# Kernel optimization log

Hardware: AMD Instinct MI355X
Metric: run time of the kernel (lower is better)

Reference implementation:

```python
import jax, jax.numpy as jnp
import numpy as np

N_TOK, BATCH, D, MEM, H, W = 196, 64, 256, 2048, 16, 16


def setup_inputs() -> dict:
    key = jax.random.key(0)
    ks = jax.random.split(key, 9)
    w_scale = 1.0 / np.sqrt(D)  # ~ Linear default init scale
    return {
        "input_tokens": jax.random.normal(ks[0], (N_TOK, BATCH, D), jnp.float32),
        "ch_memory": jax.random.normal(ks[1], (MEM, D), jnp.float32) * 0.1,
        "ch_wq": jax.random.normal(ks[2], (D, D), jnp.float32) * w_scale,
        "ch_wk": jax.random.normal(ks[3], (D, D), jnp.float32) * w_scale,
        "ch_wv": jax.random.normal(ks[4], (D, D), jnp.float32) * w_scale,
        "sp_memory": jax.random.normal(ks[5], (MEM, H, W), jnp.float32) * 0.1,
        "sp_wq": jax.random.normal(ks[6], (D, D), jnp.float32) * w_scale,
        "sp_wk": jax.random.normal(ks[7], (D, D), jnp.float32) * w_scale,
        "sp_wv": jax.random.normal(ks[8], (D, D), jnp.float32) * w_scale,
    }


def reference(input_tokens, ch_memory, ch_wq, ch_wk, ch_wv,
              sp_memory, sp_wq, sp_wk, sp_wv):
    n_tok, batch, d = input_tokens.shape
    hw = d  # spatial branch requires feature_dim == H*W
    x = input_tokens.reshape(n_tok * batch, d)  # [NB, D]

    # ---- Channel memory branch: dot-product softmax read ----
    q = x @ ch_wq.T                       # [NB, D]
    k = ch_memory @ ch_wk.T               # [M, D]
    v = ch_memory @ ch_wv.T               # [M, D]
    scores = (q @ k.T) * (1.0 / jnp.sqrt(jnp.float32(d)))  # [NB, M]
    att_c = jax.nn.softmax(scores, axis=-1)
    out_c = att_c @ v                     # [NB, D]

    # ---- Spatial memory branch: SSIM-score softmax read ----
    mem_flat = sp_memory.reshape(sp_memory.shape[0], hw)  # [M, HW]
    qf = x @ sp_wq.T                      # [NB, HW]
    kf = mem_flat @ sp_wk.T               # [M, HW]
    vf = mem_flat @ sp_wv.T               # [M, HW]

    q_mean = jnp.mean(qf, axis=1, keepdims=True)          # [NB, 1]
    k_mean = jnp.mean(kf, axis=1, keepdims=True)          # [M, 1]
    q_var = jnp.var(qf, axis=1, ddof=1, keepdims=True)    # unbiased, like torch.var
    k_var = jnp.var(kf, axis=1, ddof=1, keepdims=True)
    cov = ((qf - q_mean) @ (kf - k_mean).T) / jnp.float32(hw - 1)  # [NB, M]

    c1, c2 = 0.01, 0.03
    mean_prod = q_mean @ k_mean.T                          # [NB, M]
    numerator = (2.0 * mean_prod + c1) * (2.0 * cov + c2)
    denominator = (q_mean ** 2 + (k_mean.T) ** 2 + c1) * (q_var + k_var.T + c2)
    ssim = numerator / (denominator + 1e-8)                # [NB, M]

    att_s = jax.nn.softmax(ssim, axis=-1)
    out_s = att_s @ vf                     # [NB, HW] == [NB, D]

    return (out_c + out_s).reshape(n_tok, batch, d)
```

## Files before the change

### kernel.cpp

```cpp
#include <hip/hip_runtime.h>

#define NBQ 12544
#define DM  256
#define MM  2048

typedef __attribute__((ext_vector_type(8)))  __bf16 bf16x8;
typedef __attribute__((ext_vector_type(4)))  float  floatx4;

__device__ __forceinline__ ushort f2bf(float x) {
    unsigned u = __float_as_uint(x);
    u += 0x7fffu + ((u >> 16) & 1u);
    return (ushort)(u >> 16);
}
__device__ __forceinline__ float bf2f(ushort h) {
    return __uint_as_float(((unsigned)h) << 16);
}

__global__ __launch_bounds__(256) void gemm_proj_all(
    const float* __restrict__ x,      const float* __restrict__ ch_mem,
    const float* __restrict__ ch_wq,  const float* __restrict__ ch_wk,
    const float* __restrict__ ch_wv,  const float* __restrict__ sp_mem,
    const float* __restrict__ sp_wq,  const float* __restrict__ sp_wk,
    const float* __restrict__ sp_wv,
    ushort* __restrict__ Qb,  ushort* __restrict__ QFb,
    ushort* __restrict__ Kb,  ushort* __restrict__ KFb,
    ushort* __restrict__ Vtb, ushort* __restrict__ VFtb)
{
    __shared__ ushort As[64][72];
    __shared__ ushort W1s[64][72];
    __shared__ ushort W2s[64][72];

    int bid = blockIdx.x;
    const float* A; const float* W1; const float* W2;
    ushort* C1; ushort* C2; int nrows, trans2;
    if (bid < 784) {
        A = x; W1 = ch_wq; W2 = sp_wq; C1 = Qb; C2 = QFb; nrows = NBQ; trans2 = 0;
    } else if (bid < 912) {
        A = ch_mem; W1 = ch_wk; W2 = ch_wv; C1 = Kb; C2 = Vtb;
        nrows = MM; trans2 = 1; bid -= 784;
    } else {
        A = sp_mem; W1 = sp_wk; W2 = sp_wv; C1 = KFb; C2 = VFtb;
        nrows = MM; trans2 = 1; bid -= 912;
    }
    const int r0 = (bid >> 2) * 64;
    const int c0 = (bid & 3) * 64;

    const int tid  = threadIdx.x;
    const int wv   = tid >> 6;
    const int lane = tid & 63;
    const int quad = lane >> 4;
    const int l16  = lane & 15;
    const int rw = (wv & 1) * 32;
    const int cw = (wv >> 1) * 32;

    floatx4 acc1[2][2], acc2[2][2];
    #pragma unroll
    for (int i = 0; i < 2; ++i)
        #pragma unroll
        for (int j = 0; j < 2; ++j) {
            acc1[i][j] = (floatx4){0.f, 0.f, 0.f, 0.f};
            acc2[i][j] = (floatx4){0.f, 0.f, 0.f, 0.f};
        }

    for (int d0 = 0; d0 < 256; d0 += 64) {
        __syncthreads();
        #pragma unroll
        for (int it = 0; it < 4; ++it) {
            int idx = tid + it * 256;
            int r = idx >> 4, c4 = (idx & 15) * 4;
            float4 a4 = *(const float4*)(A  + (size_t)(r0 + r) * 256 + d0 + c4);
            float4 w14 = *(const float4*)(W1 + (size_t)(c0 + r) * 256 + d0 + c4);
            float4 w24 = *(const float4*)(W2 + (size_t)(c0 + r) * 256 + d0 + c4);
            ushort4 ab, w1b, w2b;
            ab.x = f2bf(a4.x);  ab.y = f2bf(a4.y);  ab.z = f2bf(a4.z);  ab.w = f2bf(a4.w);
            w1b.x = f2bf(w14.x); w1b.y = f2bf(w14.y); w1b.z = f2bf(w14.z); w1b.w = f2bf(w14.w);
            w2b.x = f2bf(w24.x); w2b.y = f2bf(w24.y); w2b.z = f2bf(w24.z); w2b.w = f2bf(w24.w);
            *(ushort4*)&As[r][c4]  = ab;
            *(ushort4*)&W1s[r][c4] = w1b;
            *(ushort4*)&W2s[r][c4] = w2b;
        }
        __syncthreads();
        #pragma unroll
        for (int kk = 0; kk < 64; kk += 32) {
            bf16x8 aA0 = *(const bf16x8*)&As[rw + l16][kk + quad * 8];
            bf16x8 aA1 = *(const bf16x8*)&As[rw + 16 + l16][kk + quad * 8];
            bf16x8 b10 = *(const bf16x8*)&W1s[cw + l16][kk + quad * 8];
            bf16x8 b11 = *(const bf16x8*)&W1s[cw + 16 + l16][kk + quad * 8];
            bf16x8 b20 = *(const bf16x8*)&W2s[cw + l16][kk + quad * 8];
            bf16x8 b21 = *(const bf16x8*)&W2s[cw + 16 + l16][kk + quad * 8];
            acc1[0][0] = __builtin_amdgcn_mfma_f32_16x16x32_bf16(aA0, b10, acc1[0][0], 0, 0, 0);
            acc1[0][1] = __builtin_amdgcn_mfma_f32_16x16x32_bf16(aA0, b11, acc1[0][1], 0, 0, 0);
            acc1[1][0] = __builtin_amdgcn_mfma_f32_16x16x32_bf16(aA1, b10, acc1[1][0], 0, 0, 0);
            acc1[1][1] = __builtin_amdgcn_mfma_f32_16x16x32_bf16(aA1, b11, acc1[1][1], 0, 0, 0);
            acc2[0][0] = __builtin_amdgcn_mfma_f32_16x16x32_bf16(aA0, b20, acc2[0][0], 0, 0, 0);
            acc2[0][1] = __builtin_amdgcn_mfma_f32_16x16x32_bf16(aA0, b21, acc2[0][1], 0, 0, 0);
            acc2[1][0] = __builtin_amdgcn_mfma_f32_16x16x32_bf16(aA1, b20, acc2[1][0], 0, 0, 0);
            acc2[1][1] = __builtin_amdgcn_mfma_f32_16x16x32_bf16(aA1, b21, acc2[1][1], 0, 0, 0);
        }
    }

    #pragma unroll
    for (int ag = 0; ag < 2; ++ag)
        #pragma unroll
        for (int cg = 0; cg < 2; ++cg)
            #pragma unroll
            for (int i = 0; i < 4; ++i)
                C1[(size_t)(r0 + rw + ag * 16 + quad * 4 + i) * 256
                   + c0 + cw + cg * 16 + l16] = f2bf(acc1[ag][cg][i]);

    if (!trans2) {
        #pragma unroll
        for (int ag = 0; ag < 2; ++ag)
            #pragma unroll
            for (int cg = 0; cg < 2; ++cg)
                #pragma unroll
                for (int i = 0; i < 4; ++i)
                    C2[(size_t)(r0 + rw + ag * 16 + quad * 4 + i) * 256
                       + c0 + cw + cg * 16 + l16] = f2bf(acc2[ag][cg][i]);
    } else {
        __syncthreads();
        #pragma unroll
        for (int ag = 0; ag < 2; ++ag)
            #pragma unroll
            for (int cg = 0; cg < 2; ++cg)
                #pragma unroll
                for (int i = 0; i < 4; ++i)
                    W2s[cw + cg * 16 + l16][rw + ag * 16 + quad * 4 + i] = f2bf(acc2[ag][cg][i]);
        __syncthreads();
        const int col = tid >> 2;
        const int seg = (tid & 3) * 16;
        #pragma unroll
        for (int j = 0; j < 2; ++j)
            *(uint4*)(C2 + (size_t)(c0 + col) * nrows + r0 + seg + j * 8) =
                *(const uint4*)&W2s[col][seg + j * 8];
    }
}

__global__ __launch_bounds__(256) void row_stats_kf(
    const ushort* __restrict__ KFb, float* __restrict__ km, float* __restrict__ kv)
{
    const int row  = blockIdx.x * 4 + (threadIdx.x >> 6);
    const int lane = threadIdx.x & 63;
    ushort4 u = *(const ushort4*)(KFb + (size_t)row * 256 + lane * 4);
    float a = bf2f(u.x), b = bf2f(u.y), c = bf2f(u.z), d = bf2f(u.w);
    float s  = a + b + c + d;
    float ss = a * a + b * b + c * c + d * d;
    #pragma unroll
    for (int off = 32; off > 0; off >>= 1) {
        s  += __shfl_down(s, off);
        ss += __shfl_down(ss, off);
    }
    if (lane == 0) {
        float m = s * (1.f / 256.f);
        km[row] = m;
        kv[row] = (ss - 256.f * m * m) * (1.f / 255.f);
    }
}

__global__ __launch_bounds__(256, 2) void fused_attn_st(
    const ushort* __restrict__ Qb,  const ushort* __restrict__ QFb,
    const ushort* __restrict__ Kb,  const ushort* __restrict__ KFb,
    const ushort* __restrict__ Vtb, const ushort* __restrict__ VFtb,
    const float* __restrict__ km_, const float* __restrict__ kv_,
    float* __restrict__ out)
{
    __shared__ ushort SM[37376];
    ushort (*K_lds)[264]  = (ushort(*)[264])(SM);
    ushort (*KF_lds)[264] = (ushort(*)[264])(SM + 8448);
    ushort (*Vt_lds)[40]  = (ushort(*)[40])(SM + 16896);
    ushort (*VFt_lds)[40] = (ushort(*)[40])(SM + 27136);
    float* combuf = (float*)(SM + 16896);

    const int tid  = threadIdx.x;
    const int wv   = tid >> 6;
    const int lane = tid & 63;
    const int quad = lane >> 4;
    const int l16  = lane & 15;
    const int qsel = wv & 1;
    const int br   = wv >> 1;
    const int q0   = blockIdx.x * 32;

    const ushort* qsrc = br ? QFb : Qb;
    bf16x8 aQ[8];
    {
        const ushort* qp = qsrc + (size_t)(q0 + qsel * 16 + l16) * DM + quad * 8;
        #pragma unroll
        for (int s = 0; s < 8; ++s) aQ[s] = *(const bf16x8*)(qp + s * 32);
    }

    float qmv = 0.f, qvv = 0.f;
    if (br) {
        float sum = 0.f, ss = 0.f;
        #pragma unroll
        for (int s = 0; s < 8; ++s)
            #pragma unroll
            for (int j = 0; j < 8; ++j) {
                float v = (float)aQ[s][j];
                sum += v; ss += v * v;
            }
        sum += __shfl_xor(sum, 16, 64); sum += __shfl_xor(sum, 32, 64);
        ss  += __shfl_xor(ss, 16, 64);  ss  += __shfl_xor(ss, 32, 64);
        qmv = sum * (1.f / 256.f);
        qvv = (ss - 256.f * qmv * qmv) * (1.f / 255.f);
    }

    floatx4 acc[16];
    #pragma unroll
    for (int t = 0; t < 16; ++t) acc[t] = (floatx4){0.f, 0.f, 0.f, 0.f};
    float den = 0.f;

    for (int kt = 0; kt < MM; kt += 32) {
        __syncthreads();
        #pragma unroll
        for (int it = 0; it < 4; ++it) {
            int idx = tid + it * 256;
            int r = idx >> 5, c8 = (idx & 31) * 8;
            int pr = ((r & 4) << 2) | ((r >> 3) << 2) | (r & 3);
            *(uint4*)&K_lds[pr][c8]  = *(const uint4*)(Kb  + (size_t)(kt + r) * DM + c8);
            *(uint4*)&KF_lds[pr][c8] = *(const uint4*)(KFb + (size_t)(kt + r) * DM + c8);
        }
        #pragma unroll
        for (int it = 0; it < 4; ++it) {
            int idx = tid + it * 256;
            int d = idx >> 2, kc = (idx & 3) * 8;
            *(uint4*)&Vt_lds[d][kc]  = *(const uint4*)(Vtb  + (size_t)d * MM + kt + kc);
            *(uint4*)&VFt_lds[d][kc] = *(const uint4*)(VFtb + (size_t)d * MM + kt + kc);
        }
        __syncthreads();

        floatx4 S0 = (floatx4){0.f, 0.f, 0.f, 0.f};
        floatx4 S1 = (floatx4){0.f, 0.f, 0.f, 0.f};
        const ushort (*Ksrc)[264] = br ? KF_lds : K_lds;
        #pragma unroll
        for (int s = 0; s < 8; ++s) {
            bf16x8 aK0 = *(const bf16x8*)&Ksrc[l16][s * 32 + quad * 8];
            bf16x8 aK1 = *(const bf16x8*)&Ksrc[16 + l16][s * 32 + quad * 8];
            S0 = __builtin_amdgcn_mfma_f32_16x16x32_bf16(aK0, aQ[s], S0, 0, 0, 0);
            S1 = __builtin_amdgcn_mfma_f32_16x16x32_bf16(aK1, aQ[s], S1, 0, 0, 0);
        }

        float p[8];
        if (!br) {
            #pragma unroll
            for (int r = 0; r < 4; ++r) {
                p[r]     = __expf(S0[r] * 0.0625f);
                p[4 + r] = __expf(S1[r] * 0.0625f);
            }
        } else {
            floatx4 km0 = *(const floatx4*)(km_ + kt + 8 * quad);
            floatx4 km1 = *(const floatx4*)(km_ + kt + 8 * quad + 4);
            floatx4 kv0 = *(const floatx4*)(kv_ + kt + 8 * quad);
            floatx4 kv1 = *(const floatx4*)(kv_ + kt + 8 * quad + 4);
            #pragma unroll
            for (int r = 0; r < 4; ++r) {
                {
                    float mp  = qmv * km0[r];
                    float cov = (S0[r] - 256.f * mp) * (1.f / 255.f);
                    float num = (2.f * mp + 0.01f) * (2.f * cov + 0.03f);
                    float dn  = (qmv * qmv + km0[r] * km0[r] + 0.01f) * (qvv + kv0[r] + 0.03f);
                    p[r] = __expf(num / (dn + 1e-8f));
                }
                {
                    float mp  = qmv * km1[r];
                    float cov = (S1[r] - 256.f * mp) * (1.f / 255.f);
                    float num = (2.f * mp + 0.01f) * (2.f * cov + 0.03f);
                    float dn  = (qmv * qmv + km1[r] * km1[r] + 0.01f) * (qvv + kv1[r] + 0.03f);
                    p[4 + r] = __expf(num / (dn + 1e-8f));
                }
            }
        }
        union { ushort u[8]; bf16x8 v; } ap;
        #pragma unroll
        for (int j = 0; j < 8; ++j) {
            den += p[j];
            ap.u[j] = f2bf(p[j]);
        }

        const ushort (*Vsrc)[40] = br ? VFt_lds : Vt_lds;
        #pragma unroll
        for (int t = 0; t < 16; ++t) {
            bf16x8 bV = *(const bf16x8*)&Vsrc[t * 16 + l16][quad * 8];
            acc[t] = __builtin_amdgcn_mfma_f32_16x16x32_bf16(ap.v, bV, acc[t], 0, 0, 0);
        }
    }

    den += __shfl_xor(den, 16, 64);
    den += __shfl_xor(den, 32, 64);
    float rdn[4];
    #pragma unroll
    for (int r = 0; r < 4; ++r)
        rdn[r] = 1.f / __shfl(den, quad * 4 + r, 64);

    __syncthreads();
    if (br) {
        #pragma unroll
        for (int t = 0; t < 16; ++t)
            #pragma unroll
            for (int r = 0; r < 4; ++r)
                combuf[(qsel * 16 + quad * 4 + r) * 256 + t * 16 + l16] = acc[t][r] * rdn[r];
    }
    __syncthreads();
    if (!br) {
        #pragma unroll
        for (int t = 0; t < 16; ++t)
            #pragma unroll
            for (int r = 0; r < 4; ++r) {
                int ql = qsel * 16 + quad * 4 + r;
                out[(size_t)(q0 + ql) * DM + t * 16 + l16] =
                    acc[t][r] * rdn[r] + combuf[ql * 256 + t * 16 + l16];
            }
    }
}

extern "C" void kernel_launch(void* const* d_in, const int* in_sizes, int n_in,
                              void* d_out, int out_size, void* d_ws, size_t ws_size,
                              hipStream_t stream)
{
    const float* x      = (const float*)d_in[0];
    const float* ch_mem = (const float*)d_in[1];
    const float* ch_wq  = (const float*)d_in[2];
    const float* ch_wk  = (const float*)d_in[3];
    const float* ch_wv  = (const float*)d_in[4];
    const float* sp_mem = (const float*)d_in[5];
    const float* sp_wq  = (const float*)d_in[6];
    const float* sp_wk  = (const float*)d_in[7];
    const float* sp_wv  = (const float*)d_in[8];
    float* out = (float*)d_out;

    ushort* Qb   = (ushort*)d_ws;
    ushort* QFb  = Qb   + (size_t)NBQ * DM;
    ushort* Kb   = QFb  + (size_t)NBQ * DM;
    ushort* KFb  = Kb   + (size_t)MM * DM;
    ushort* Vtb  = KFb  + (size_t)MM * DM;
    ushort* VFtb = Vtb  + (size_t)MM * DM;
    float*  km   = (float*)(VFtb + (size_t)MM * DM);
    float*  kv   = km + MM;

    dim3 blk(256);
    gemm_proj_all<<<dim3(1040), blk, 0, stream>>>(
        x, ch_mem, ch_wq, ch_wk, ch_wv, sp_mem, sp_wq, sp_wk, sp_wv,
        Qb, QFb, Kb, KFb, Vtb, VFtb);
    row_stats_kf<<<dim3(MM / 4), blk, 0, stream>>>(KFb, km, kv);
    fused_attn_st<<<dim3(NBQ / 32), blk, 0, stream>>>(
        Qb, QFb, Kb, KFb, Vtb, VFtb, km, kv, out);
}
```

Baseline: 267.0 us.

## Fuse key row statistics into projection kernel with full-width row blocks

The projection kernel now gives each block 64 rows across all 256 output columns. The bf16 A tile is staged once in LDS and reused across the four column chunks, where before it was reloaded per column tile. For the spatial-memory keys, per-row sum and sum of squares are reduced from the accumulators inside the kernel, so the separate row_stats kernel and its launch go away. The grid shrinks from 1040 to 260 larger blocks, which lowers parallelism on the GPU. The stats now come from fp32 accumulators instead of the bf16-rounded stored values.

Measured after the change: 269.9 us. No clear change (+1.1%).

```diff
diff --git a/kernel.cpp b/kernel.cpp
--- a/kernel.cpp
+++ b/kernel.cpp
@@ -16,34 +16,37 @@
     return __uint_as_float(((unsigned)h) << 16);
 }
 
-__global__ __launch_bounds__(256) void gemm_proj_all(
+__global__ __launch_bounds__(256) void proj_stats(
     const float* __restrict__ x,      const float* __restrict__ ch_mem,
-    const float* __restrict__ ch_wq,  const float* __restrict__ ch_wk,
-    const float* __restrict__ ch_wv,  const float* __restrict__ sp_mem,
-    const float* __restrict__ sp_wq,  const float* __restrict__ sp_wk,
-    const float* __restrict__ sp_wv,
+    const float* __restrict__ sp_mem,
+    const float* __restrict__ ch_wq,  const float* __restrict__ sp_wq,
+    const float* __restrict__ ch_wk,  const float* __restrict__ ch_wv,
+    const float* __restrict__ sp_wk,  const float* __restrict__ sp_wv,
     ushort* __restrict__ Qb,  ushort* __restrict__ QFb,
     ushort* __restrict__ Kb,  ushort* __restrict__ KFb,
-    ushort* __restrict__ Vtb, ushort* __restrict__ VFtb)
+    ushort* __restrict__ Vtb, ushort* __restrict__ VFtb,
+    float* __restrict__ km,   float* __restrict__ kv)
 {
-    __shared__ ushort As[64][72];
+    __shared__ ushort As[64][264];
     __shared__ ushort W1s[64][72];
     __shared__ ushort W2s[64][72];
+    __shared__ float  sbuf[4][4][8];
+    __shared__ float  ssbuf[4][4][8];
 
     int bid = blockIdx.x;
     const float* A; const float* W1; const float* W2;
-    ushort* C1; ushort* C2; int nrows, trans2;
-    if (bid < 784) {
-        A = x; W1 = ch_wq; W2 = sp_wq; C1 = Qb; C2 = QFb; nrows = NBQ; trans2 = 0;
-    } else if (bid < 912) {
+    ushort* C1; ushort* C2; int nrows, trans2, dostats;
+    if (bid < 196) {
+        A = x; W1 = ch_wq; W2 = sp_wq; C1 = Qb; C2 = QFb;
+        nrows = NBQ; trans2 = 0; dostats = 0;
+    } else if (bid < 228) {
         A = ch_mem; W1 = ch_wk; W2 = ch_wv; C1 = Kb; C2 = Vtb;
-        nrows = MM; trans2 = 1; bid -= 784;
+        nrows = MM; trans2 = 1; dostats = 0; bid -= 196;
     } else {
         A = sp_mem; W1 = sp_wk; W2 = sp_wv; C1 = KFb; C2 = VFtb;
-        nrows = MM; trans2 = 1; bid -= 912;
-    }
-    const int r0 = (bid >> 2) * 64;
-    const int c0 = (bid & 3) * 64;
+        nrows = MM; trans2 = 1; dostats = 1; bid -= 228;
+    }
+    const int r0 = bid * 64;
 
     const int tid  = threadIdx.x;
     const int wv   = tid >> 6;
@@ -53,107 +56,148 @@
     const int rw = (wv & 1) * 32;
     const int cw = (wv >> 1) * 32;
 
-    floatx4 acc1[2][2], acc2[2][2];
     #pragma unroll
-    for (int i = 0; i < 2; ++i)
-        #pragma unroll
-        for (int j = 0; j < 2; ++j) {
-            acc1[i][j] = (floatx4){0.f, 0.f, 0.f, 0.f};
-            acc2[i][j] = (floatx4){0.f, 0.f, 0.f, 0.f};
-        }
-
-    for (int d0 = 0; d0 < 256; d0 += 64) {
-        __syncthreads();
-        #pragma unroll
-        for (int it = 0; it < 4; ++it) {
-            int idx = tid + it * 256;
-            int r = idx >> 4, c4 = (idx & 15) * 4;
-            float4 a4 = *(const float4*)(A  + (size_t)(r0 + r) * 256 + d0 + c4);
-            float4 w14 = *(const float4*)(W1 + (size_t)(c0 + r) * 256 + d0 + c4);
-            float4 w24 = *(const float4*)(W2 + (size_t)(c0 + r) * 256 + d0 + c4);
-            ushort4 ab, w1b, w2b;
-            ab.x = f2bf(a4.x);  ab.y = f2bf(a4.y);  ab.z = f2bf(a4.z);  ab.w = f2bf(a4.w);
-            w1b.x = f2bf(w14.x); w1b.y = f2bf(w14.y); w1b.z = f2bf(w14.z); w1b.w = f2bf(w14.w);
-            w2b.x = f2bf(w24.x); w2b.y = f2bf(w24.y); w2b.z = f2bf(w24.z); w2b.w = f2bf(w24.w);
-            *(ushort4*)&As[r][c4]  = ab;
-            *(ushort4*)&W1s[r][c4] = w1b;
-            *(ushort4*)&W2s[r][c4] = w2b;
-        }
-        __syncthreads();
-        #pragma unroll
-        for (int kk = 0; kk < 64; kk += 32) {
-            bf16x8 aA0 = *(const bf16x8*)&As[rw + l16][kk + quad * 8];
-            bf16x8 aA1 = *(const bf16x8*)&As[rw + 16 + l16][kk + quad * 8];
-            bf16x8 b10 = *(const bf16x8*)&W1s[cw + l16][kk + quad * 8];
-            bf16x8 b11 = *(const bf16x8*)&W1s[cw + 16 + l16][kk + quad * 8];
-            bf16x8 b20 = *(const bf16x8*)&W2s[cw + l16][kk + quad * 8];
-            bf16x8 b21 = *(const bf16x8*)&W2s[cw + 16 + l16][kk + quad * 8];
-            acc1[0][0] = __builtin_amdgcn_mfma_f32_16x16x32_bf16(aA0, b10, acc1[0][0], 0, 0, 0);
-            acc1[0][1] = __builtin_amdgcn_mfma_f32_16x16x32_bf16(aA0, b11, acc1[0][1], 0, 0, 0);
-            acc1[1][0] = __builtin_amdgcn_mfma_f32_16x16x32_bf16(aA1, b10, acc1[1][0], 0, 0, 0);
-            acc1[1][1] = __builtin_amdgcn_mfma_f32_16x16x32_bf16(aA1, b11, acc1[1][1], 0, 0, 0);
-            acc2[0][0] = __builtin_amdgcn_mfma_f32_16x16x32_bf16(aA0, b20, acc2[0][0], 0, 0, 0);
-            acc2[0][1] = __builtin_amdgcn_mfma_f32_16x16x32_bf16(aA0, b21, acc2[0][1], 0, 0, 0);
-            acc2[1][0] = __builtin_amdgcn_mfma_f32_16x16x32_bf16(aA1, b20, acc2[1][0], 0, 0, 0);
-            acc2[1][1] = __builtin_amdgcn_mfma_f32_16x16x32_bf16(aA1, b21, acc2[1][1], 0, 0, 0);
-        }
-    }
-
-    #pragma unroll
-    for (int ag = 0; ag < 2; ++ag)
-        #pragma unroll
-        for (int cg = 0; cg < 2; ++cg)
-            #pragma unroll
-            for (int i = 0; i < 4; ++i)
-                C1[(size_t)(r0 + rw + ag * 16 + quad * 4 + i) * 256
-                   + c0 + cw + cg * 16 + l16] = f2bf(acc1[ag][cg][i]);
-
-    if (!trans2) {
+    for (int it = 0; it < 8; ++it) {
+        int idx = tid + it * 256;
+        int r = idx >> 5, c8 = (idx & 31) * 8;
+        const float* ap = A + (size_t)(r0 + r) * 256 + c8;
+        float4 a0 = *(const float4*)ap;
+        float4 a1 = *(const float4*)(ap + 4);
+        ushort4 b0, b1;
+        b0.x = f2bf(a0.x); b0.y = f2bf(a0.y); b0.z = f2bf(a0.z); b0.w = f2bf(a0.w);
+        b1.x = f2bf(a1.x); b1.y = f2bf(a1.y); b1.z = f2bf(a1.z); b1.w = f2bf(a1.w);
+        *(ushort4*)&As[r][c8]     = b0;
+        *(ushort4*)&As[r][c8 + 4] = b1;
+    }
+
+    float s8[8]  = {0.f, 0.f, 0.f, 0.f, 0.f, 0.f, 0.f, 0.f};
+    float ss8[8] = {0.f, 0.f, 0.f, 0.f, 0.f, 0.f, 0.f, 0.f};
+
+    for (int c0 = 0; c0 < 256; c0 += 64) {
+        floatx4 acc1[2][2], acc2[2][2];
+        #pragma unroll
+        for (int i = 0; i < 2; ++i)
+            #pragma unroll
+            for (int j = 0; j < 2; ++j) {
+                acc1[i][j] = (floatx4){0.f, 0.f, 0.f, 0.f};
+                acc2[i][j] = (floatx4){0.f, 0.f, 0.f, 0.f};
+            }
+
+        for (int d0 = 0; d0 < 256; d0 += 64) {
+            __syncthreads();
+            #pragma unroll
+            for (int it = 0; it < 4; ++it) {
+                int idx = tid + it * 256;
+                int which = idx >> 9;
+                int rem = idx & 511;
+                int r = rem >> 3, c8 = (rem & 7) * 8;
+                const float* wp = (which ? W2 : W1) + (size_t)(c0 + r) * 256 + d0 + c8;
+                float4 w0 = *(const float4*)wp;
+                float4 w1 = *(const float4*)(wp + 4);
+                ushort4 b0, b1;
+                b0.x = f2bf(w0.x); b0.y = f2bf(w0.y); b0.z = f2bf(w0.z); b0.w = f2bf(w0.w);
+                b1.x = f2bf(w1.x); b1.y = f2bf(w1.y); b1.z = f2bf(w1.z); b1.w = f2bf(w1.w);
+                ushort* dst = which ? &W2s[r][c8] : &W1s[r][c8];
+                *(ushort4*)dst       = b0;
+                *(ushort4*)(dst + 4) = b1;
+            }
+            __syncthreads();
+            #pragma unroll
+            for (int kk = 0; kk < 64; kk += 32) {
+                bf16x8 aA0 = *(const bf16x8*)&As[rw + l16][d0 + kk + quad * 8];
+                bf16x8 aA1 = *(const bf16x8*)&As[rw + 16 + l16][d0 + kk + quad * 8];
+                bf16x8 b10 = *(const bf16x8*)&W1s[cw + l16][kk + quad * 8];
+                bf16x8 b11 = *(const bf16x8*)&W1s[cw + 16 + l16][kk + quad * 8];
+                bf16x8 b20 = *(const bf16x8*)&W2s[cw + l16][kk + quad * 8];
+                bf16x8 b21 = *(const bf16x8*)&W2s[cw + 16 + l16][kk + quad * 8];
+                acc1[0][0] = __builtin_amdgcn_mfma_f32_16x16x32_bf16(aA0, b10, acc1[0][0], 0, 0, 0);
+                acc1[0][1] = __builtin_amdgcn_mfma_f32_16x16x32_bf16(aA0, b11, acc1[0][1], 0, 0, 0);
+                acc1[1][0] = __builtin_amdgcn_mfma_f32_16x16x32_bf16(aA1, b10, acc1[1][0], 0, 0, 0);
+                acc1[1][1] = __builtin_amdgcn_mfma_f32_16x16x32_bf16(aA1, b11, acc1[1][1], 0, 0, 0);
+                acc2[0][0] = __builtin_amdgcn_mfma_f32_16x16x32_bf16(aA0, b20, acc2[0][0], 0, 0, 0);
+                acc2[0][1] = __builtin_amdgcn_mfma_f32_16x16x32_bf16(aA0, b21, acc2[0][1], 0, 0, 0);
+                acc2[1][0] = __builtin_amdgcn_mfma_f32_16x16x32_bf16(aA1, b20, acc2[1][0], 0, 0, 0);
+                acc2[1][1] = __builtin_amdgcn_mfma_f32_16x16x32_bf16(aA1, b21, acc2[1][1], 0, 0, 0);
+            }
+        }
+
+        if (dostats) {
+            #pragma unroll
+            for (int ag = 0; ag < 2; ++ag)
+                #pragma unroll
+                for (int i = 0; i < 4; ++i) {
+                    float v0 = acc1[ag][0][i], v1 = acc1[ag][1][i];
+                    s8[ag * 4 + i]  += v0 + v1;
+                    ss8[ag * 4 + i] += v0 * v0 + v1 * v1;
+                }
+        }
+
         #pragma unroll
         for (int ag = 0; ag < 2; ++ag)
             #pragma unroll
             for (int cg = 0; cg < 2; ++cg)
                 #pragma unroll
                 for (int i = 0; i < 4; ++i)
-                    C2[(size_t)(r0 + rw + ag * 16 + quad * 4 + i) * 256
-                       + c0 + cw + cg * 16 + l16] = f2bf(acc2[ag][cg][i]);
-    } else {
+                    C1[(size_t)(r0 + rw + ag * 16 + quad * 4 + i) * 256
+                       + c0 + cw + cg * 16 + l16] = f2bf(acc1[ag][cg][i]);
+
+        if (!trans2) {
+            #pragma unroll
+            for (int ag = 0; ag < 2; ++ag)
+                #pragma unroll
+                for (int cg = 0; cg < 2; ++cg)
+                    #pragma unroll
+                    for (int i = 0; i < 4; ++i)
+                        C2[(size_t)(r0 + rw + ag * 16 + quad * 4 + i) * 256
+                           + c0 + cw + cg * 16 + l16] = f2bf(acc2[ag][cg][i]);
+        } else {
+            __syncthreads();
+            #pragma unroll
+            for (int ag = 0; ag < 2; ++ag)
+                #pragma unroll
+                for (int cg = 0; cg < 2; ++cg)
+                    #pragma unroll
+                    for (int i = 0; i < 4; ++i)
+                        W2s[cw + cg * 16 + l16][rw + ag * 16 + quad * 4 + i] =
+                            f2bf(acc2[ag][cg][i]);
+            __syncthreads();
+            const int col = tid >> 2;
+            const int seg = (tid & 3) * 16;
+            #pragma unroll
+            for (int j = 0; j < 2; ++j)
+                *(uint4*)(C2 + (size_t)(c0 + col) * nrows + r0 + seg + j * 8) =
+                    *(const uint4*)&W2s[col][seg + j * 8];
+        }
+    }
+
+    if (dostats) {
+        #pragma unroll
+        for (int k = 0; k < 8; ++k) {
+            #pragma unroll
+            for (int m = 1; m < 16; m <<= 1) {
+                s8[k]  += __shfl_xor(s8[k], m, 64);
+                ss8[k] += __shfl_xor(ss8[k], m, 64);
+            }
+        }
+        if (l16 == 0) {
+            #pragma unroll
+            for (int k = 0; k < 8; ++k) {
+                sbuf[wv][quad][k]  = s8[k];
+                ssbuf[wv][quad][k] = ss8[k];
+            }
+        }
         __syncthreads();
-        #pragma unroll
-        for (int ag = 0; ag < 2; ++ag)
-            #pragma unroll
-            for (int cg = 0; cg < 2; ++cg)
-                #pragma unroll
-                for (int i = 0; i < 4; ++i)
-                    W2s[cw + cg * 16 + l16][rw + ag * 16 + quad * 4 + i] = f2bf(acc2[ag][cg][i]);
-        __syncthreads();
-        const int col = tid >> 2;
-        const int seg = (tid & 3) * 16;
-        #pragma unroll
-        for (int j = 0; j < 2; ++j)
-            *(uint4*)(C2 + (size_t)(c0 + col) * nrows + r0 + seg + j * 8) =
-                *(const uint4*)&W2s[col][seg + j * 8];
-    }
-}
-
-__global__ __launch_bounds__(256) void row_stats_kf(
-    const ushort* __restrict__ KFb, float* __restrict__ km, float* __restrict__ kv)
-{
-    const int row  = blockIdx.x * 4 + (threadIdx.x >> 6);
-    const int lane = threadIdx.x & 63;
-    ushort4 u = *(const ushort4*)(KFb + (size_t)row * 256 + lane * 4);
-    float a = bf2f(u.x), b = bf2f(u.y), c = bf2f(u.z), d = bf2f(u.w);
-    float s  = a + b + c + d;
-    float ss = a * a + b * b + c * c + d * d;
-    #pragma unroll
-    for (int off = 32; off > 0; off >>= 1) {
-        s  += __shfl_down(s, off);
-        ss += __shfl_down(ss, off);
-    }
-    if (lane == 0) {
-        float m = s * (1.f / 256.f);
-        km[row] = m;
-        kv[row] = (ss - 256.f * m * m) * (1.f / 255.f);
+        if (tid < 64) {
+            int rl = tid;
+            int wvb  = rl >> 5;
+            int qd   = (rl >> 2) & 3;
+            int idx8 = ((rl >> 4) & 1) * 4 + (rl & 3);
+            float s  = sbuf[wvb][qd][idx8]  + sbuf[2 + wvb][qd][idx8];
+            float ss = ssbuf[wvb][qd][idx8] + ssbuf[2 + wvb][qd][idx8];
+            float m = s * (1.f / 256.f);
+            km[r0 + rl] = m;
+            kv[r0 + rl] = (ss - 256.f * m * m) * (1.f / 255.f);
+        }
     }
 }
 
@@ -337,10 +381,9 @@
     float*  kv   = km + MM;
 
     dim3 blk(256);
-    gemm_proj_all<<<dim3(1040), blk, 0, stream>>>(
-        x, ch_mem, ch_wq, ch_wk, ch_wv, sp_mem, sp_wq, sp_wk, sp_wv,
-        Qb, QFb, Kb, KFb, Vtb, VFtb);
-    row_stats_kf<<<dim3(MM / 4), blk, 0, stream>>>(KFb, km, kv);
+    proj_stats<<<dim3(260), blk, 0, stream>>>(
+        x, ch_mem, sp_mem, ch_wq, sp_wq, ch_wk, ch_wv, sp_wk, sp_wv,
+        Qb, QFb, Kb, KFb, Vtb, VFtb, km, kv);
     fused_attn_st<<<dim3(NBQ / 32), blk, 0, stream>>>(
         Qb, QFb, Kb, KFb, Vtb, VFtb, km, kv, out);
 }
```
